# Kernel optimization log

Measured on AMD Instinct MI355X. Metric: run time of the kernel, lower is better.

Reference implementation:

```python
import jax, jax.numpy as jnp
import numpy as np

BS, DIM, N, M, O = 2048, 32, 40, 40, 200


def setup_inputs() -> dict:
    key = jax.random.key(0)
    k1, k2, k3 = jax.random.split(key, 3)
    x = jax.random.normal(k1, (BS, DIM, N), dtype=jnp.float32)
    y = jax.random.normal(k2, (BS, DIM, M), dtype=jnp.float32)
    # Linear(n*m -> o), no bias; scale like nn.Linear default-ish init
    W = jax.random.normal(k3, (O, N * M), dtype=jnp.float32) * (1.0 / np.sqrt(N * M))
    return {"x": x, "y": y, "W": W}


def reference(x, y, W):
    # Original math: z[b,d,n,m] = x[b,d,n] * y[b,d,m]; flatten (n,m) -> k; out = z @ W.T
    # Fused form: out[b,d,o] = sum_{n,m} x[b,d,n] * y[b,d,m] * W[o, n*M+m]
    o, nm = W.shape
    Wr = W.reshape(o, x.shape[-1], y.shape[-1])  # [O, N, M]
    return jnp.einsum('bdn,bdm,onm->bdo', x, y, Wr)
```

## Files before the change

kernel.cpp:

```cpp
#include <hip/hip_runtime.h>
#include <hip/hip_fp16.h>

#define OOv   200
#define KKv   1600
#define OPAD  208
#define NSTEPS 50
#define NSUPER 25
#define CHUNK_BYTES 13312
#define SUPER_BYTES 26624
#define XSTR 40
#define YSTR 40

typedef _Float16 half8  __attribute__((ext_vector_type(8)));
typedef _Float16 half2v __attribute__((ext_vector_type(2)));
typedef __attribute__((ext_vector_type(4))) float floatx4;

__global__ void wb_convert_kernel(const float* __restrict__ W,
                                  unsigned short* __restrict__ Wh) {
    int idx = blockIdx.x * 256 + threadIdx.x;
    if (idx >= NSTEPS * OPAD * 32) return;
    int j    = idx & 7;
    int slot = (idx >> 3) % (OPAD * 4);
    int t    = (idx >> 3) / (OPAD * 4);
    int o    = slot >> 2;
    int kgs  = slot & 3;
    int kg   = kgs ^ ((o >> 1) & 3);
    int k    = (4 * (t / 5) + kg) * 40 + 8 * (t % 5) + j;
    float v  = (o < OOv) ? W[o * KKv + k] : 0.0f;
    union { _Float16 h; unsigned short u; } cv; cv.h = (_Float16)v;
    Wh[idx] = cv.u;
}

__global__ __launch_bounds__(512, 4) void cin_mfma_kernel(
        const float* __restrict__ X, const float* __restrict__ Y,
        const unsigned short* __restrict__ Wh, float* __restrict__ Out) {
    __shared__ __align__(16) unsigned char bsm[2 * SUPER_BYTES];
    __shared__ __align__(16) _Float16 xlds[64 * XSTR];
    __shared__ __align__(16) _Float16 ylds[64 * YSTR];

    const int tid    = threadIdx.x;
    const int wave   = tid >> 6;
    const int lane   = tid & 63;
    const int li     = lane & 15;
    const int kg     = lane >> 4;
    const int rowgrp = wave & 1;
    const int colgrp = wave >> 1;

    static const int nt_t[4]  = {4, 3, 3, 3};
    static const int cbt_t[4] = {0, 4, 7, 10};
    const int nt  = nt_t[colgrp];
    const int cbt = cbt_t[colgrp];
    const long blockbase = (long)blockIdx.x * 64;

    const float* xg = X + blockbase * 40;
    const float* yg = Y + blockbase * 40;
    for (int i = tid; i < 640; i += 512) {
        int r  = i / 10;
        int c4 = (i % 10) * 4;
        floatx4 vx = *(const floatx4*)(xg + i * 4);
        floatx4 vy = *(const floatx4*)(yg + i * 4);
        union { half2v h[2]; unsigned long long u; } px, py;
        px.h[0] = (half2v){(_Float16)vx.x, (_Float16)vx.y};
        px.h[1] = (half2v){(_Float16)vx.z, (_Float16)vx.w};
        py.h[0] = (half2v){(_Float16)vy.x, (_Float16)vy.y};
        py.h[1] = (half2v){(_Float16)vy.z, (_Float16)vy.w};
        *(unsigned long long*)(xlds + r * XSTR + c4) = px.u;
        *(unsigned long long*)(ylds + r * YSTR + c4) = py.u;
    }
    for (int u = wave; u < 26; u += 8) {
        int off = u * 1024 + lane * 16;
        __builtin_amdgcn_global_load_lds(
            (const __attribute__((address_space(1))) unsigned int*)((const char*)Wh + off),
            (__attribute__((address_space(3))) unsigned int*)(bsm + off),
            16, 0, 0);
    }
    __syncthreads();

    half8 yr[2][5];
#pragma unroll
    for (int rt = 0; rt < 2; ++rt) {
        int row = rowgrp * 32 + rt * 16 + li;
#pragma unroll
        for (int p = 0; p < 5; ++p)
            yr[rt][p] = *(const half8*)(ylds + row * YSTR + p * 8);
    }

    floatx4 acc[2][4];
#pragma unroll
    for (int rt = 0; rt < 2; ++rt)
#pragma unroll
        for (int ct = 0; ct < 4; ++ct)
            acc[rt][ct] = (floatx4){0.f, 0.f, 0.f, 0.f};

    const int bfoff = (cbt * 16 + li) * 64 + ((kg ^ ((li >> 1) & 3)) * 16);

    for (int mg = 0; mg < 5; ++mg) {
        half2v xs[2][2];
#pragma unroll
        for (int w = 0; w < 2; ++w)
#pragma unroll
            for (int rt = 0; rt < 2; ++rt) {
                _Float16 xv = xlds[(rowgrp * 32 + rt * 16 + li) * XSTR
                                   + (2 * mg + w) * 4 + kg];
                xs[w][rt] = (half2v){xv, xv};
            }

#pragma unroll
        for (int ss5 = 0; ss5 < 5; ++ss5) {
            const int sstep = mg * 5 + ss5;
            if (sstep + 1 < NSUPER) {
                const char* src = (const char*)Wh + (size_t)(sstep + 1) * SUPER_BYTES;
                unsigned char* dst = bsm + ((sstep + 1) & 1) * SUPER_BYTES;
                for (int u = wave; u < 26; u += 8) {
                    int off = u * 1024 + lane * 16;
                    __builtin_amdgcn_global_load_lds(
                        (const __attribute__((address_space(1))) unsigned int*)(src + off),
                        (__attribute__((address_space(3))) unsigned int*)(dst + off),
                        16, 0, 0);
                }
            }
            const unsigned char* cbuf = bsm + (sstep & 1) * SUPER_BYTES;

#pragma unroll
            for (int h = 0; h < 2; ++h) {
                const int t = 2 * sstep + h;
                const int p = t % 5;
                const int w = (t / 5) & 1;
                const unsigned char* chunk = cbuf + h * CHUNK_BYTES;

                half8 bf[4];
#pragma unroll
                for (int ct = 0; ct < 4; ++ct)
                    if (ct < nt)
                        bf[ct] = *(const half8*)(chunk + bfoff + ct * 1024);

                half8 af[2];
#pragma unroll
                for (int rt = 0; rt < 2; ++rt) {
                    half8 xsp = __builtin_shufflevector(xs[w][rt], xs[w][rt],
                                                        0, 1, 0, 1, 0, 1, 0, 1);
                    af[rt] = xsp * yr[rt][p];
                }

#pragma unroll
                for (int ct = 0; ct < 4; ++ct)
                    if (ct < nt)
#pragma unroll
                        for (int rt = 0; rt < 2; ++rt)
                            acc[rt][ct] = __builtin_amdgcn_mfma_f32_16x16x32_f16(
                                af[rt], bf[ct], acc[rt][ct], 0, 0, 0);
            }
            __syncthreads();
        }
    }

#pragma unroll
    for (int rt = 0; rt < 2; ++rt) {
#pragma unroll
        for (int ct = 0; ct < 4; ++ct) {
            if (ct >= nt) continue;
            int gcol = (cbt + ct) * 16 + li;
            if (gcol < OOv) {
#pragma unroll
                for (int r4 = 0; r4 < 4; ++r4) {
                    long grow = blockbase + rowgrp * 32 + rt * 16 + kg * 4 + r4;
                    Out[grow * OOv + gcol] = acc[rt][ct][r4];
                }
            }
        }
    }
}

extern "C" void kernel_launch(void* const* d_in, const int* in_sizes, int n_in,
                              void* d_out, int out_size, void* d_ws, size_t ws_size,
                              hipStream_t stream) {
    (void)in_sizes; (void)n_in; (void)out_size; (void)ws_size;
    const float* X = (const float*)d_in[0];
    const float* Y = (const float*)d_in[1];
    const float* W = (const float*)d_in[2];
    float* Out = (float*)d_out;
    unsigned short* Wh = (unsigned short*)d_ws;

    wb_convert_kernel<<<1300, 256, 0, stream>>>(W, Wh);
    cin_mfma_kernel<<<1024, 512, 0, stream>>>(X, Y, Wh, Out);
}
```

Baseline: 130.1 us.

## Switch to 32x32x16 MFMA with 128-row blocks and register-resident X/Y operands

Replaces the 16x16x32 MFMA tiling with 32x32x16 MFMA tiles. Each block now covers 128 rows instead of 64, halving the grid and doubling how often each W tile is reused. X and Y are loaded directly from global memory into registers, with X prefetched one step ahead, which removes the LDS staging buffers. W is relaid out into larger super-steps covering 7 padded column tiles (224 outputs), so there are fewer barriers per row block. The tradeoff is more padding waste on the last column group, higher register pressure from the 16-wide accumulators, and only 512 blocks to fill the GPU.

```diff
diff --git a/kernel.cpp b/kernel.cpp
--- a/kernel.cpp
+++ b/kernel.cpp
@@ -3,29 +3,27 @@
 
 #define OOv   200
 #define KKv   1600
-#define OPAD  208
-#define NSTEPS 50
-#define NSUPER 25
-#define CHUNK_BYTES 13312
-#define SUPER_BYTES 26624
-#define XSTR 40
-#define YSTR 40
+#define OTILES 7
+#define TSTEPS 100
+#define NMG   20
+#define STEP_BYTES 7168
+#define SUPER_BYTES 35840
 
 typedef _Float16 half8  __attribute__((ext_vector_type(8)));
 typedef _Float16 half2v __attribute__((ext_vector_type(2)));
-typedef __attribute__((ext_vector_type(4))) float floatx4;
+typedef __attribute__((ext_vector_type(4)))  float floatx4;
+typedef __attribute__((ext_vector_type(16))) float floatx16;
 
 __global__ void wb_convert_kernel(const float* __restrict__ W,
                                   unsigned short* __restrict__ Wh) {
     int idx = blockIdx.x * 256 + threadIdx.x;
-    if (idx >= NSTEPS * OPAD * 32) return;
+    if (idx >= TSTEPS * 224 * 16) return;
     int j    = idx & 7;
-    int slot = (idx >> 3) % (OPAD * 4);
-    int t    = (idx >> 3) / (OPAD * 4);
-    int o    = slot >> 2;
-    int kgs  = slot & 3;
-    int kg   = kgs ^ ((o >> 1) & 3);
-    int k    = (4 * (t / 5) + kg) * 40 + 8 * (t % 5) + j;
+    int slot = (idx >> 3) % 448;
+    int t    = (idx >> 3) / 448;
+    int o    = slot >> 1;
+    int h    = slot & 1;
+    int k    = (2 * (t / 5) + h) * 40 + 8 * (t % 5) + j;
     float v  = (o < OOv) ? W[o * KKv + k] : 0.0f;
     union { _Float16 h; unsigned short u; } cv; cv.h = (_Float16)v;
     Wh[idx] = cv.u;
@@ -35,136 +33,114 @@
         const float* __restrict__ X, const float* __restrict__ Y,
         const unsigned short* __restrict__ Wh, float* __restrict__ Out) {
     __shared__ __align__(16) unsigned char bsm[2 * SUPER_BYTES];
-    __shared__ __align__(16) _Float16 xlds[64 * XSTR];
-    __shared__ __align__(16) _Float16 ylds[64 * YSTR];
 
-    const int tid    = threadIdx.x;
-    const int wave   = tid >> 6;
-    const int lane   = tid & 63;
-    const int li     = lane & 15;
-    const int kg     = lane >> 4;
-    const int rowgrp = wave & 1;
-    const int colgrp = wave >> 1;
+    const int tid     = threadIdx.x;
+    const int wave    = tid >> 6;
+    const int lane    = tid & 63;
+    const int c32     = lane & 31;
+    const int h       = lane >> 5;
+    const int rowhalf = wave & 1;
+    const int colgrp  = wave >> 1;
+    const int nt      = (colgrp == 3) ? 1 : 2;
+    const int cbt     = colgrp * 2;
+    const long blockbase = (long)blockIdx.x * 128;
 
-    static const int nt_t[4]  = {4, 3, 3, 3};
-    static const int cbt_t[4] = {0, 4, 7, 10};
-    const int nt  = nt_t[colgrp];
-    const int cbt = cbt_t[colgrp];
-    const long blockbase = (long)blockIdx.x * 64;
+    const long row0 = blockbase + rowhalf * 64 + c32;
+    const long row1 = row0 + 32;
 
-    const float* xg = X + blockbase * 40;
-    const float* yg = Y + blockbase * 40;
-    for (int i = tid; i < 640; i += 512) {
-        int r  = i / 10;
-        int c4 = (i % 10) * 4;
-        floatx4 vx = *(const floatx4*)(xg + i * 4);
-        floatx4 vy = *(const floatx4*)(yg + i * 4);
-        union { half2v h[2]; unsigned long long u; } px, py;
-        px.h[0] = (half2v){(_Float16)vx.x, (_Float16)vx.y};
-        px.h[1] = (half2v){(_Float16)vx.z, (_Float16)vx.w};
-        py.h[0] = (half2v){(_Float16)vy.x, (_Float16)vy.y};
-        py.h[1] = (half2v){(_Float16)vy.z, (_Float16)vy.w};
-        *(unsigned long long*)(xlds + r * XSTR + c4) = px.u;
-        *(unsigned long long*)(ylds + r * YSTR + c4) = py.u;
-    }
-    for (int u = wave; u < 26; u += 8) {
+    for (int u = wave; u < 35; u += 8) {
         int off = u * 1024 + lane * 16;
         __builtin_amdgcn_global_load_lds(
             (const __attribute__((address_space(1))) unsigned int*)((const char*)Wh + off),
             (__attribute__((address_space(3))) unsigned int*)(bsm + off),
             16, 0, 0);
     }
+
+    half2v yr[2][5][4];
+#pragma unroll
+    for (int r = 0; r < 2; ++r) {
+        const float* yp = Y + (r ? row1 : row0) * 40;
+#pragma unroll
+        for (int p = 0; p < 5; ++p) {
+            floatx4 a = *(const floatx4*)(yp + p * 8);
+            floatx4 b = *(const floatx4*)(yp + p * 8 + 4);
+            yr[r][p][0] = (half2v){(_Float16)a.x, (_Float16)a.y};
+            yr[r][p][1] = (half2v){(_Float16)a.z, (_Float16)a.w};
+            yr[r][p][2] = (half2v){(_Float16)b.x, (_Float16)b.y};
+            yr[r][p][3] = (half2v){(_Float16)b.z, (_Float16)b.w};
+        }
+    }
+    float xf0 = X[row0 * 40 + h];
+    float xf1 = X[row1 * 40 + h];
+
     __syncthreads();
 
-    half8 yr[2][5];
-#pragma unroll
-    for (int rt = 0; rt < 2; ++rt) {
-        int row = rowgrp * 32 + rt * 16 + li;
-#pragma unroll
-        for (int p = 0; p < 5; ++p)
-            yr[rt][p] = *(const half8*)(ylds + row * YSTR + p * 8);
-    }
-
-    floatx4 acc[2][4];
+    floatx16 acc[2][2];
 #pragma unroll
     for (int rt = 0; rt < 2; ++rt)
 #pragma unroll
-        for (int ct = 0; ct < 4; ++ct)
-            acc[rt][ct] = (floatx4){0.f, 0.f, 0.f, 0.f};
+        for (int ct = 0; ct < 2; ++ct)
+            acc[rt][ct] = (floatx16)0.f;
 
-    const int bfoff = (cbt * 16 + li) * 64 + ((kg ^ ((li >> 1) & 3)) * 16);
+    const int bfoff = (c32 * 2 + h) * 16;
 
-    for (int mg = 0; mg < 5; ++mg) {
-        half2v xs[2][2];
-#pragma unroll
-        for (int w = 0; w < 2; ++w)
-#pragma unroll
-            for (int rt = 0; rt < 2; ++rt) {
-                _Float16 xv = xlds[(rowgrp * 32 + rt * 16 + li) * XSTR
-                                   + (2 * mg + w) * 4 + kg];
-                xs[w][rt] = (half2v){xv, xv};
+    for (int mg = 0; mg < NMG; ++mg) {
+        half2v xs0 = (half2v){(_Float16)xf0, (_Float16)xf0};
+        half2v xs1 = (half2v){(_Float16)xf1, (_Float16)xf1};
+        if (mg + 1 < NMG) {
+            xf0 = X[row0 * 40 + 2 * (mg + 1) + h];
+            xf1 = X[row1 * 40 + 2 * (mg + 1) + h];
+        }
+        if (mg + 1 < NMG) {
+            const char* src = (const char*)Wh + (size_t)(mg + 1) * SUPER_BYTES;
+            unsigned char* dst = bsm + ((mg + 1) & 1) * SUPER_BYTES;
+            for (int u = wave; u < 35; u += 8) {
+                int off = u * 1024 + lane * 16;
+                __builtin_amdgcn_global_load_lds(
+                    (const __attribute__((address_space(1))) unsigned int*)(src + off),
+                    (__attribute__((address_space(3))) unsigned int*)(dst + off),
+                    16, 0, 0);
             }
+        }
+        const unsigned char* cbuf = bsm + (mg & 1) * SUPER_BYTES;
 
 #pragma unroll
-        for (int ss5 = 0; ss5 < 5; ++ss5) {
-            const int sstep = mg * 5 + ss5;
-            if (sstep + 1 < NSUPER) {
-                const char* src = (const char*)Wh + (size_t)(sstep + 1) * SUPER_BYTES;
-                unsigned char* dst = bsm + ((sstep + 1) & 1) * SUPER_BYTES;
-                for (int u = wave; u < 26; u += 8) {
-                    int off = u * 1024 + lane * 16;
-                    __builtin_amdgcn_global_load_lds(
-                        (const __attribute__((address_space(1))) unsigned int*)(src + off),
-                        (__attribute__((address_space(3))) unsigned int*)(dst + off),
-                        16, 0, 0);
-                }
-            }
-            const unsigned char* cbuf = bsm + (sstep & 1) * SUPER_BYTES;
+        for (int p = 0; p < 5; ++p) {
+            const unsigned char* chunk = cbuf + p * STEP_BYTES;
 
+            half8 bf[2];
 #pragma unroll
-            for (int h = 0; h < 2; ++h) {
-                const int t = 2 * sstep + h;
-                const int p = t % 5;
-                const int w = (t / 5) & 1;
-                const unsigned char* chunk = cbuf + h * CHUNK_BYTES;
+            for (int ct = 0; ct < 2; ++ct)
+                if (ct < nt)
+                    bf[ct] = *(const half8*)(chunk + (cbt + ct) * 1024 + bfoff);
 
-                half8 bf[4];
+            union { half8 v8; half2v h2[4]; } af;
 #pragma unroll
-                for (int ct = 0; ct < 4; ++ct)
-                    if (ct < nt)
-                        bf[ct] = *(const half8*)(chunk + bfoff + ct * 1024);
-
-                half8 af[2];
+            for (int q = 0; q < 4; ++q) af.h2[q] = xs0 * yr[0][p][q];
+            acc[0][0] = __builtin_amdgcn_mfma_f32_32x32x16_f16(af.v8, bf[0], acc[0][0], 0, 0, 0);
+            if (nt > 1)
+                acc[0][1] = __builtin_amdgcn_mfma_f32_32x32x16_f16(af.v8, bf[1], acc[0][1], 0, 0, 0);
 #pragma unroll
-                for (int rt = 0; rt < 2; ++rt) {
-                    half8 xsp = __builtin_shufflevector(xs[w][rt], xs[w][rt],
-                                                        0, 1, 0, 1, 0, 1, 0, 1);
-                    af[rt] = xsp * yr[rt][p];
-                }
-
-#pragma unroll
-                for (int ct = 0; ct < 4; ++ct)
-                    if (ct < nt)
-#pragma unroll
-                        for (int rt = 0; rt < 2; ++rt)
-                            acc[rt][ct] = __builtin_amdgcn_mfma_f32_16x16x32_f16(
-                                af[rt], bf[ct], acc[rt][ct], 0, 0, 0);
-            }
-            __syncthreads();
+            for (int q = 0; q < 4; ++q) af.h2[q] = xs1 * yr[1][p][q];
+            acc[1][0] = __builtin_amdgcn_mfma_f32_32x32x16_f16(af.v8, bf[0], acc[1][0], 0, 0, 0);
+            if (nt > 1)
+                acc[1][1] = __builtin_amdgcn_mfma_f32_32x32x16_f16(af.v8, bf[1], acc[1][1], 0, 0, 0);
         }
+        __syncthreads();
     }
 
 #pragma unroll
     for (int rt = 0; rt < 2; ++rt) {
 #pragma unroll
-        for (int ct = 0; ct < 4; ++ct) {
+        for (int ct = 0; ct < 2; ++ct) {
             if (ct >= nt) continue;
-            int gcol = (cbt + ct) * 16 + li;
+            int gcol = (cbt + ct) * 32 + c32;
             if (gcol < OOv) {
 #pragma unroll
-                for (int r4 = 0; r4 < 4; ++r4) {
-                    long grow = blockbase + rowgrp * 32 + rt * 16 + kg * 4 + r4;
-                    Out[grow * OOv + gcol] = acc[rt][ct][r4];
+                for (int reg = 0; reg < 16; ++reg) {
+                    long grow = blockbase + rowhalf * 64 + rt * 32
+                              + (reg & 3) + 8 * (reg >> 2) + 4 * h;
+                    Out[grow * OOv + gcol] = acc[rt][ct][reg];
                 }
             }
         }
@@ -181,6 +157,6 @@
     float* Out = (float*)d_out;
     unsigned short* Wh = (unsigned short*)d_ws;
 
-    wb_convert_kernel<<<1300, 256, 0, stream>>>(W, Wh);
-    cin_mfma_kernel<<<1024, 512, 0, stream>>>(X, Y, Wh, Out);
+    wb_convert_kernel<<<1400, 256, 0, stream>>>(W, Wh);
+    cin_mfma_kernel<<<512, 512, 0, stream>>>(X, Y, Wh, Out);
 }
```

Result: slower. 144.4 us (+11.0%).
